# Kernel optimization log

Measured on AMD Instinct MI355X. Metric: run time of the kernel, lower is better.

Reference implementation:

```python
import jax, jax.numpy as jnp
import numpy as np

D_K = 128


def setup_inputs() -> dict:
    key = jax.random.key(0)
    ks = jax.random.split(key, 10)
    B, S, D, TP, TE, DK = 4, 4096, 1024, 16, 64, D_K
    sc = lambda fan_in: 1.0 / np.sqrt(fan_in)
    return {
        "x": jax.random.normal(ks[0], (B, S, D), jnp.float32),
        "time_points": jax.random.normal(ks[1], (B, TP, TE), jnp.float32),
        "Wq": jax.random.normal(ks[2], (D, DK), jnp.float32) * sc(D),
        "bq": jnp.zeros((DK,), jnp.float32),
        "Wk": jax.random.normal(ks[3], (D, DK), jnp.float32) * sc(D),
        "bk": jnp.zeros((DK,), jnp.float32),
        "Wv": jax.random.normal(ks[4], (D, DK), jnp.float32) * sc(D),
        "bv": jnp.zeros((DK,), jnp.float32),
        "Wt": jax.random.normal(ks[5], (TE, DK), jnp.float32) * sc(TE),
        "bt": jnp.zeros((DK,), jnp.float32),
    }


def reference(x, time_points, Wq, bq, Wk, bk, Wv, bv, Wt, bt):
    B, S, _ = x.shape
    Q = x @ Wq + bq              # [B,S,dk]
    K = x @ Wk + bk              # [B,S,dk]
    V = x @ Wv + bv              # [B,S,dk]
    E = time_points @ Wt + bt    # [B,TP,dk] = time_emb
    # T = repeat(E, S times along dim 1). Then T^T @ T = S * E^T E and
    # ||T||_F = sqrt(S) * ||E||_F, so we never materialize T.
    S_f = jnp.asarray(S, jnp.float32)
    EtE = jnp.einsum('btd,bte->bde', E, E)            # [B,dk,dk]
    T_norm = jnp.sqrt(S_f * jnp.sum(E * E, axis=(1, 2), keepdims=False))  # [B]
    T_scaled = (S_f * EtE) / (T_norm[:, None, None] + 1e-8)  # [B,dk,dk]
    QT = jnp.einsum('bsd,bde->bse', Q, T_scaled)      # [B,S,dk]
    scores = jnp.einsum('bse,bte->bst', QT, K)        # [B,S,S]
    scores = scores / jnp.sqrt(jnp.asarray(D_K, jnp.float32))
    attn = jax.nn.softmax(scores, axis=-1)            # [B,S,S]
    out = jnp.einsum('bst,btd->bsd', attn, V)         # [B,S,dk]
    return out, attn
```

## Files before the change

### kernel.cpp

```cpp
#include <hip/hip_runtime.h>
#include <math.h>

#define BB 4
#define SS 4096
#define DD 1024
#define TPp 16
#define TEe 64
#define DKk 128

typedef __attribute__((ext_vector_type(8))) short short8;
typedef __attribute__((ext_vector_type(4))) float floatx4;
typedef __attribute__((ext_vector_type(16))) float floatx16;

#define BSTRIDE 524288
#define WFRAG 131072
#define XTILE 32768

static __device__ inline short f2bf(float f) {
  union { float f; unsigned u; } v; v.f = f;
  unsigned r = v.u + 0x7fff + ((v.u >> 16) & 1);
  return (short)(r >> 16);
}
static __device__ inline float bf2f(short s) {
  union { unsigned u; float f; } v; v.u = ((unsigned)(unsigned short)s) << 16;
  return v.f;
}

__global__ __launch_bounds__(256) void temb_kernel(const float* __restrict__ tp,
                                                   const float* __restrict__ Wt,
                                                   const float* __restrict__ bt,
                                                   const float* __restrict__ bq,
                                                   float* __restrict__ Tws,
                                                   float* __restrict__ bqtws) {
  __shared__ float sE[TPp * DKk];
  __shared__ float sB[TPp];
  __shared__ float red[256];
  const int p = blockIdx.x, b = blockIdx.y;
  const int tid = threadIdx.x;
  float lsq = 0.f;
  for (int l = 0; l < 8; ++l) {
    int idx = tid + 256 * l;
    int i = idx >> 7, j = idx & 127;
    float a = bt[j];
    for (int c = 0; c < TEe; ++c)
      a += tp[((size_t)b * TPp + i) * TEe + c] * Wt[c * DKk + j];
    sE[idx] = a;
    lsq += a * a;
  }
  red[tid] = lsq;
  __syncthreads();
  for (int s2 = 128; s2 > 0; s2 >>= 1) {
    if (tid < s2) red[tid] += red[tid + s2];
    __syncthreads();
  }
  const float total = red[0];
  const float scale = (float)SS / (sqrtf((float)SS * total) + 1e-8f);
  if (tid < TPp) {
    float a = 0.f;
    for (int d2 = 0; d2 < DKk; ++d2) a += bq[d2] * sE[tid * DKk + d2];
    sB[tid] = a;
  }
  __syncthreads();
  for (int l = 0; l < 8; ++l) {
    int idx = p * 2048 + tid + 256 * l;
    int d2 = idx >> 7, e = idx & 127;
    float a = 0.f;
    #pragma unroll
    for (int t = 0; t < TPp; ++t) a += sE[t * DKk + d2] * sE[t * DKk + e];
    Tws[(size_t)b * DKk * DKk + idx] = scale * a;
  }
  if (p == 0 && tid < DKk) {
    float a = 0.f;
    #pragma unroll
    for (int t = 0; t < TPp; ++t) a += sB[t] * sE[t * DKk + tid];
    bqtws[b * DKk + tid] = scale * a;
  }
}

__global__ __launch_bounds__(128) void wqp_kernel(const float* __restrict__ Wq,
                                                  const float* __restrict__ Tws,
                                                  short* __restrict__ WqphF,
                                                  short* __restrict__ WqplF) {
  __shared__ float sW[DKk];
  const int m = blockIdx.x, b = blockIdx.y;
  const int e = threadIdx.x;
  sW[e] = Wq[(size_t)m * DKk + e];
  __syncthreads();
  const float* Tb = Tws + (size_t)b * DKk * DKk;
  float a = 0.f;
  #pragma unroll 8
  for (int d2 = 0; d2 < DKk; ++d2) a += sW[d2] * Tb[d2 * DKk + e];
  const size_t off = (size_t)b * WFRAG +
      (size_t)((e >> 5) * 64 + (m >> 4)) * 512 + (32 * ((m >> 3) & 1) + (e & 31)) * 8 +
      (m & 7);
  short hh = f2bf(a);
  WqphF[off] = hh;
  WqplF[off] = f2bf(a - bf2f(hh));
}

__global__ __launch_bounds__(256) void wcast_kernel(const float* __restrict__ Wk,
                                                    const float* __restrict__ Wv,
                                                    short* __restrict__ WkhF,
                                                    short* __restrict__ WklF,
                                                    short* __restrict__ WvhF,
                                                    short* __restrict__ WvlF) {
  const float* W = blockIdx.y ? Wv : Wk;
  short* H = blockIdx.y ? WvhF : WkhF;
  short* L = blockIdx.y ? WvlF : WklF;
  const int ks = blockIdx.x;
  const int wave = threadIdx.x >> 6, lane = threadIdx.x & 63;
  const int n = wave * 32 + (lane & 31);
  const int k0 = ks * 16 + (lane >> 5) * 8;
  short8 h, l;
  #pragma unroll
  for (int j = 0; j < 8; ++j) {
    float v = W[(size_t)(k0 + j) * DKk + n];
    short hh = f2bf(v);
    h[j] = hh;
    l[j] = f2bf(v - bf2f(hh));
  }
  const size_t off = ((size_t)wave * 64 + ks) * 512 + lane * 8;
  *(short8*)&H[off] = h;
  *(short8*)&L[off] = l;
}

__global__ __launch_bounds__(256) void xcast_kernel(const float* __restrict__ x,
                                                    short* __restrict__ XAh,
                                                    short* __restrict__ XAl) {
  const int tileG = blockIdx.x;
  const int rowbase = tileG * 32;
  const int tid = threadIdx.x;
  const int t = tid & 31, khalf = (tid >> 5) & 1, w = tid >> 6;
  const size_t abase = (size_t)tileG * XTILE + (size_t)(tid & 63) * 8;
  const float* xr = x + (size_t)(rowbase + t) * DD + khalf * 8;
  #pragma unroll
  for (int it = 0; it < 16; ++it) {
    const int ks = it * 4 + w;
    float4 u0 = *(const float4*)(xr + ks * 16);
    float4 u1 = *(const float4*)(xr + ks * 16 + 4);
    const float v[8] = {u0.x, u0.y, u0.z, u0.w, u1.x, u1.y, u1.z, u1.w};
    short8 h, l;
    #pragma unroll
    for (int j = 0; j < 8; ++j) {
      short hh = f2bf(v[j]);
      h[j] = hh;
      l[j] = f2bf(v[j] - bf2f(hh));
    }
    *(short8*)&XAh[abase + (size_t)ks * 512] = h;
    *(short8*)&XAl[abase + (size_t)ks * 512] = l;
  }
}

__global__ __launch_bounds__(256, 4) void proj_kernel(const short* __restrict__ XAh,
                                                      const short* __restrict__ XAl,
                                                      const short* __restrict__ WqphF,
                                                      const short* __restrict__ WqplF,
                                                      const short* __restrict__ WkhF,
                                                      const short* __restrict__ WklF,
                                                      const short* __restrict__ WvhF,
                                                      const short* __restrict__ WvlF,
                                                      const float* __restrict__ bqt,
                                                      const float* __restrict__ bk,
                                                      const float* __restrict__ bv,
                                                      short* __restrict__ QTh,
                                                      short* __restrict__ QTl,
                                                      short* __restrict__ Kh,
                                                      short* __restrict__ Kl,
                                                      short* __restrict__ VT) {
  const int id = blockIdx.x;
  const int region = id >> 9, tileG = id & 511;
  const int b = tileG >> 7, tileL = tileG & 127;
  const int tid = threadIdx.x, wave = tid >> 6, lane = tid & 63;
  const int l31 = lane & 31, half = lane >> 5;
  const short* BH;
  const short* BL;
  if (region == 0)      { BH = WqphF + (size_t)b * WFRAG; BL = WqplF + (size_t)b * WFRAG; }
  else if (region == 1) { BH = WkhF; BL = WklF; }
  else                  { BH = WvhF; BL = WvlF; }
  BH += (size_t)wave * 32768 + (size_t)lane * 8;
  BL += (size_t)wave * 32768 + (size_t)lane * 8;
  const short* AH = XAh + (size_t)tileG * XTILE + (size_t)lane * 8;
  const short* AL = XAl + (size_t)tileG * XTILE + (size_t)lane * 8;
  floatx16 accE, accO;
  #pragma unroll
  for (int r = 0; r < 16; ++r) { accE[r] = 0.f; accO[r] = 0.f; }
  for (int ks = 0; ks < 64; ks += 2) {
    short8 a0h = *(const short8*)(AH + (size_t)ks * 512);
    short8 a0l = *(const short8*)(AL + (size_t)ks * 512);
    short8 b0h = *(const short8*)(BH + (size_t)ks * 512);
    short8 b0l = *(const short8*)(BL + (size_t)ks * 512);
    short8 a1h = *(const short8*)(AH + (size_t)(ks + 1) * 512);
    short8 a1l = *(const short8*)(AL + (size_t)(ks + 1) * 512);
    short8 b1h = *(const short8*)(BH + (size_t)(ks + 1) * 512);
    short8 b1l = *(const short8*)(BL + (size_t)(ks + 1) * 512);
    accE = __builtin_amdgcn_mfma_f32_32x32x16_bf16(a0l, b0h, accE, 0, 0, 0);
    accO = __builtin_amdgcn_mfma_f32_32x32x16_bf16(a1l, b1h, accO, 0, 0, 0);
    accE = __builtin_amdgcn_mfma_f32_32x32x16_bf16(a0h, b0l, accE, 0, 0, 0);
    accO = __builtin_amdgcn_mfma_f32_32x32x16_bf16(a1h, b1l, accO, 0, 0, 0);
    accE = __builtin_amdgcn_mfma_f32_32x32x16_bf16(a0h, b0h, accE, 0, 0, 0);
    accO = __builtin_amdgcn_mfma_f32_32x32x16_bf16(a1h, b1h, accO, 0, 0, 0);
  }
  floatx16 acc;
  #pragma unroll
  for (int r = 0; r < 16; ++r) acc[r] = accE[r] + accO[r];
  const int f = wave * 32 + l31;
  if (region <= 1) {
    short* Hp = (region == 0) ? QTh : Kh;
    short* Lp = (region == 0) ? QTl : Kl;
    const float bias = (region == 0) ? bqt[b * DKk + f] : bk[f];
    const int fks = f >> 4, fh = (f >> 3) & 1, fj = f & 7;
    const size_t qkbase =
        (size_t)b * BSTRIDE + (size_t)tileL * 4096 + (size_t)fks * 512 + fj;
    #pragma unroll
    for (int reg = 0; reg < 16; ++reg) {
      const int t = (reg & 3) + 8 * (reg >> 2) + 4 * half;
      const size_t off = qkbase + (size_t)(fh * 32 + t) * 8;
      float v = acc[reg] + bias;
      short hh = f2bf(v);
      Hp[off] = hh;
      Lp[off] = f2bf(v - bf2f(hh));
    }
  } else {
    const float biasv = bv[f];
    #pragma unroll
    for (int g = 0; g < 4; ++g) {
      short4 s4;
      s4.x = f2bf(acc[4 * g + 0] + biasv);
      s4.y = f2bf(acc[4 * g + 1] + biasv);
      s4.z = f2bf(acc[4 * g + 2] + biasv);
      s4.w = f2bf(acc[4 * g + 3] + biasv);
      const size_t off = (size_t)b * BSTRIDE +
          (size_t)(wave * 256 + tileL * 2 + (g >> 1)) * 512 +
          (size_t)((g & 1) * 32 + l31) * 8 + 4 * half;
      *(short4*)&VT[off] = s4;
    }
  }
}

__global__ __launch_bounds__(256, 2) void ml_kernel(const short* __restrict__ QTh,
                                                    const short* __restrict__ QTl,
                                                    const short* __restrict__ Kh,
                                                    const short* __restrict__ Kl,
                                                    float* __restrict__ mrow,
                                                    float* __restrict__ linv) {
  __shared__ float smM[4][32], smL[4][32];
  const int id = blockIdx.x;
  const int xcd = id & 7;
  const int b = xcd >> 1;
  const int tile = ((id >> 3) << 1) + (xcd & 1);
  const int rowbase = tile * 32;
  const int tid = threadIdx.x;
  const int wave = tid >> 6, lane = tid & 63;
  const int l31 = lane & 31;
  const float sc = 0.088388347648318447f;
  const size_t qbase = (size_t)b * BSTRIDE + (size_t)tile * 4096 + lane * 8;
  short8 qh[8], ql[8];
  #pragma unroll
  for (int ks = 0; ks < 8; ++ks) {
    qh[ks] = *(const short8*)(QTh + qbase + ks * 512);
    ql[ks] = *(const short8*)(QTl + qbase + ks * 512);
  }
  float m = -INFINITY, l = 0.f;
  for (int ct = wave; ct < 128; ct += 4) {
    const size_t kbase = (size_t)b * BSTRIDE + (size_t)ct * 4096 + lane * 8;
    floatx16 accA, accB;
    #pragma unroll
    for (int r = 0; r < 16; ++r) { accA[r] = 0.f; accB[r] = 0.f; }
    #pragma unroll
    for (int ks = 0; ks < 4; ++ks) {
      short8 kh0 = *(const short8*)(Kh + kbase + ks * 512);
      short8 kl0 = *(const short8*)(Kl + kbase + ks * 512);
      short8 kh1 = *(const short8*)(Kh + kbase + (ks + 4) * 512);
      short8 kl1 = *(const short8*)(Kl + kbase + (ks + 4) * 512);
      accA = __builtin_amdgcn_mfma_f32_32x32x16_bf16(kh0, qh[ks], accA, 0, 0, 0);
      accB = __builtin_amdgcn_mfma_f32_32x32x16_bf16(kh1, qh[ks + 4], accB, 0, 0, 0);
      accA = __builtin_amdgcn_mfma_f32_32x32x16_bf16(kh0, ql[ks], accA, 0, 0, 0);
      accB = __builtin_amdgcn_mfma_f32_32x32x16_bf16(kh1, ql[ks + 4], accB, 0, 0, 0);
      accA = __builtin_amdgcn_mfma_f32_32x32x16_bf16(kl0, qh[ks], accA, 0, 0, 0);
      accB = __builtin_amdgcn_mfma_f32_32x32x16_bf16(kl1, qh[ks + 4], accB, 0, 0, 0);
    }
    float s[16];
    float tmax = -INFINITY;
    #pragma unroll
    for (int r = 0; r < 16; ++r) {
      s[r] = (accA[r] + accB[r]) * sc;
      tmax = fmaxf(tmax, s[r]);
    }
    const float mn = fmaxf(m, tmax);
    float ps = 0.f;
    #pragma unroll
    for (int r = 0; r < 16; ++r) ps += __expf(s[r] - mn);
    l = l * __expf(m - mn) + ps;
    m = mn;
  }
  {
    const float mo = __shfl_xor(m, 32, 64);
    const float lo = __shfl_xor(l, 32, 64);
    const float mn = fmaxf(m, mo);
    l = l * __expf(m - mn) + lo * __expf(mo - mn);
    m = mn;
  }
  if (lane < 32) { smM[wave][l31] = m; smL[wave][l31] = l; }
  __syncthreads();
  if (tid < 32) {
    float mm = smM[0][tid], ll = smL[0][tid];
    #pragma unroll
    for (int w = 1; w < 4; ++w) {
      const float mo = smM[w][tid], lo = smL[w][tid];
      const float mn = fmaxf(mm, mo);
      ll = ll * __expf(mm - mn) + lo * __expf(mo - mn);
      mm = mn;
    }
    mrow[b * SS + rowbase + tid] = mm;
    linv[b * SS + rowbase + tid] = 1.0f / ll;
  }
}

__global__ __launch_bounds__(256, 2) void pv_kernel(const short* __restrict__ QTh,
                                                    const short* __restrict__ QTl,
                                                    const short* __restrict__ Kh,
                                                    const short* __restrict__ Kl,
                                                    const short* __restrict__ VT,
                                                    float* __restrict__ attn,
                                                    const float* __restrict__ mrow,
                                                    const float* __restrict__ linv,
                                                    float* __restrict__ outp) {
  __shared__ float sAcc[3][4][64][16];
  const int id = blockIdx.x;
  const int xcd = id & 7;
  const int b = xcd >> 1;
  const int tile = ((id >> 3) << 1) + (xcd & 1);
  const int rowbase = tile * 32;
  const int tid = threadIdx.x;
  const int wave = tid >> 6, lane = tid & 63;
  const int l31 = lane & 31, half = lane >> 5;
  const float sc = 0.088388347648318447f;
  const size_t qbase = (size_t)b * BSTRIDE + (size_t)tile * 4096 + lane * 8;
  short8 qh[8], ql[8];
  #pragma unroll
  for (int ks = 0; ks < 8; ++ks) {
    qh[ks] = *(const short8*)(QTh + qbase + ks * 512);
    ql[ks] = *(const short8*)(QTl + qbase + ks * 512);
  }
  const float m_i = mrow[b * SS + rowbase + l31];
  const float li = linv[b * SS + rowbase + l31];
  float* arow = attn + (size_t)b * SS * SS + (size_t)(rowbase + l31) * SS + 4 * half;
  const short* vtb = VT + (size_t)b * BSTRIDE + lane * 8;
  floatx16 pacc[4];
  #pragma unroll
  for (int dt = 0; dt < 4; ++dt)
    #pragma unroll
    for (int r = 0; r < 16; ++r) pacc[dt][r] = 0.f;
  for (int ct = wave; ct < 128; ct += 4) {
    const size_t kbase = (size_t)b * BSTRIDE + (size_t)ct * 4096 + lane * 8;
    floatx16 accA, accB;
    #pragma unroll
    for (int r = 0; r < 16; ++r) { accA[r] = 0.f; accB[r] = 0.f; }
    #pragma unroll
    for (int ks = 0; ks < 4; ++ks) {
      short8 kh0 = *(const short8*)(Kh + kbase + ks * 512);
      short8 kl0 = *(const short8*)(Kl + kbase + ks * 512);
      short8 kh1 = *(const short8*)(Kh + kbase + (ks + 4) * 512);
      short8 kl1 = *(const short8*)(Kl + kbase + (ks + 4) * 512);
      accA = __builtin_amdgcn_mfma_f32_32x32x16_bf16(kh0, qh[ks], accA, 0, 0, 0);
      accB = __builtin_amdgcn_mfma_f32_32x32x16_bf16(kh1, qh[ks + 4], accB, 0, 0, 0);
      accA = __builtin_amdgcn_mfma_f32_32x32x16_bf16(kh0, ql[ks], accA, 0, 0, 0);
      accB = __builtin_amdgcn_mfma_f32_32x32x16_bf16(kh1, ql[ks + 4], accB, 0, 0, 0);
      accA = __builtin_amdgcn_mfma_f32_32x32x16_bf16(kl0, qh[ks], accA, 0, 0, 0);
      accB = __builtin_amdgcn_mfma_f32_32x32x16_bf16(kl1, qh[ks + 4], accB, 0, 0, 0);
    }
    float p[16];
    #pragma unroll
    for (int r = 0; r < 16; ++r)
      p[r] = __expf((accA[r] + accB[r]) * sc - m_i) * li;
    #pragma unroll
    for (int g = 0; g < 4; ++g) {
      floatx4 o = {p[4 * g], p[4 * g + 1], p[4 * g + 2], p[4 * g + 3]};
      __builtin_nontemporal_store(o, (floatx4*)(arow + ct * 32 + 8 * g));
    }
    short8 af0, af1;
    #pragma unroll
    for (int rr = 0; rr < 4; ++rr) {
      const float shl = __shfl_xor(p[rr], 32, 64);
      const float shh = __shfl_xor(p[rr + 4], 32, 64);
      af0[rr] = f2bf(half ? shh : p[rr]);
      af0[rr + 4] = f2bf(half ? p[rr + 4] : shl);
      const float shl2 = __shfl_xor(p[rr + 8], 32, 64);
      const float shh2 = __shfl_xor(p[rr + 12], 32, 64);
      af1[rr] = f2bf(half ? shh2 : p[rr + 8]);
      af1[rr + 4] = f2bf(half ? p[rr + 12] : shl2);
    }
    #pragma unroll
    for (int dt = 0; dt < 4; ++dt) {
      short8 v0 = *(const short8*)(vtb + (size_t)(dt * 256 + ct * 2) * 512);
      pacc[dt] = __builtin_amdgcn_mfma_f32_32x32x16_bf16(af0, v0, pacc[dt], 0, 0, 0);
      short8 v1 = *(const short8*)(vtb + (size_t)(dt * 256 + ct * 2 + 1) * 512);
      pacc[dt] = __builtin_amdgcn_mfma_f32_32x32x16_bf16(af1, v1, pacc[dt], 0, 0, 0);
    }
  }
  if (wave > 0) {
    #pragma unroll
    for (int dt = 0; dt < 4; ++dt)
      #pragma unroll
      for (int r = 0; r < 16; ++r) sAcc[wave - 1][dt][lane][r] = pacc[dt][r];
  }
  __syncthreads();
  if (wave == 0) {
    #pragma unroll
    for (int dt = 0; dt < 4; ++dt)
      #pragma unroll
      for (int r = 0; r < 16; ++r) {
        const int q = (r & 3) + 8 * (r >> 2) + 4 * half;
        const float v = pacc[dt][r] + sAcc[0][dt][lane][r] + sAcc[1][dt][lane][r] +
                        sAcc[2][dt][lane][r];
        outp[((size_t)b * SS + rowbase + q) * DKk + dt * 32 + l31] = v;
      }
  }
}

extern "C" void kernel_launch(void* const* d_in, const int* in_sizes, int n_in,
                              void* d_out, int out_size, void* d_ws, size_t ws_size,
                              hipStream_t stream) {
  const float* x  = (const float*)d_in[0];
  const float* tp = (const float*)d_in[1];
  const float* Wq = (const float*)d_in[2];
  const float* bq = (const float*)d_in[3];
  const float* Wk = (const float*)d_in[4];
  const float* bk = (const float*)d_in[5];
  const float* Wv = (const float*)d_in[6];
  const float* bv = (const float*)d_in[7];
  const float* Wt = (const float*)d_in[8];
  const float* bt = (const float*)d_in[9];
  float* out  = (float*)d_out;
  float* attn = out + (size_t)BB * SS * DKk;
  float* ws = (float*)d_ws;
  float* Tws   = ws;
  float* bqt   = ws + 65536;
  short* WqphF = (short*)(ws + 66048);
  short* WqplF = (short*)(ws + 328192);
  short* WkhF  = (short*)(ws + 590336);
  short* WklF  = (short*)(ws + 655872);
  short* WvhF  = (short*)(ws + 721408);
  short* WvlF  = (short*)(ws + 786944);
  short* XAh   = (short*)(ws + 852480);
  short* XAl   = (short*)(ws + 9241088);
  short* QTh   = (short*)(ws + 17629696);
  short* QTl   = (short*)(ws + 18678272);
  short* Kh    = (short*)(ws + 19726848);
  short* Kl    = (short*)(ws + 20775424);
  short* VT    = (short*)(ws + 21824000);
  float* mrow  = ws + 22872576;
  float* lin   = ws + 22888960;

  temb_kernel<<<dim3(8, 4), 256, 0, stream>>>(tp, Wt, bt, bq, Tws, bqt);
  wqp_kernel<<<dim3(1024, 4), 128, 0, stream>>>(Wq, Tws, WqphF, WqplF);
  wcast_kernel<<<dim3(64, 2), 256, 0, stream>>>(Wk, Wv, WkhF, WklF, WvhF, WvlF);
  xcast_kernel<<<512, 256, 0, stream>>>(x, XAh, XAl);
  proj_kernel<<<1536, 256, 0, stream>>>(XAh, XAl, WqphF, WqplF, WkhF, WklF,
                                        WvhF, WvlF, bqt, bk, bv,
                                        QTh, QTl, Kh, Kl, VT);
  ml_kernel<<<512, 256, 0, stream>>>(QTh, QTl, Kh, Kl, mrow, lin);
  pv_kernel<<<512, 256, 0, stream>>>(QTh, QTl, Kh, Kl, VT, attn, mrow, lin, out);
}
```

Measured before the change: 620.0 us.

## Fuse QKV projections per tile and split attention key range across blocks

```diff
diff --git a/kernel.cpp b/kernel.cpp
--- a/kernel.cpp
+++ b/kernel.cpp
@@ -151,7 +151,7 @@
   }
 }
 
-__global__ __launch_bounds__(256, 4) void proj_kernel(const short* __restrict__ XAh,
+__global__ __launch_bounds__(256, 2) void proj_kernel(const short* __restrict__ XAh,
                                                       const short* __restrict__ XAl,
                                                       const short* __restrict__ WqphF,
                                                       const short* __restrict__ WqplF,
@@ -167,73 +167,73 @@
                                                       short* __restrict__ Kh,
                                                       short* __restrict__ Kl,
                                                       short* __restrict__ VT) {
-  const int id = blockIdx.x;
-  const int region = id >> 9, tileG = id & 511;
+  const int tileG = blockIdx.x;
   const int b = tileG >> 7, tileL = tileG & 127;
   const int tid = threadIdx.x, wave = tid >> 6, lane = tid & 63;
   const int l31 = lane & 31, half = lane >> 5;
-  const short* BH;
-  const short* BL;
-  if (region == 0)      { BH = WqphF + (size_t)b * WFRAG; BL = WqplF + (size_t)b * WFRAG; }
-  else if (region == 1) { BH = WkhF; BL = WklF; }
-  else                  { BH = WvhF; BL = WvlF; }
-  BH += (size_t)wave * 32768 + (size_t)lane * 8;
-  BL += (size_t)wave * 32768 + (size_t)lane * 8;
+  const size_t woff = (size_t)wave * 32768 + (size_t)lane * 8;
+  const short* BQh = WqphF + (size_t)b * WFRAG + woff;
+  const short* BQl = WqplF + (size_t)b * WFRAG + woff;
+  const short* BKh = WkhF + woff;
+  const short* BKl = WklF + woff;
+  const short* BVh = WvhF + woff;
+  const short* BVl = WvlF + woff;
   const short* AH = XAh + (size_t)tileG * XTILE + (size_t)lane * 8;
   const short* AL = XAl + (size_t)tileG * XTILE + (size_t)lane * 8;
-  floatx16 accE, accO;
-  #pragma unroll
-  for (int r = 0; r < 16; ++r) { accE[r] = 0.f; accO[r] = 0.f; }
-  for (int ks = 0; ks < 64; ks += 2) {
-    short8 a0h = *(const short8*)(AH + (size_t)ks * 512);
-    short8 a0l = *(const short8*)(AL + (size_t)ks * 512);
-    short8 b0h = *(const short8*)(BH + (size_t)ks * 512);
-    short8 b0l = *(const short8*)(BL + (size_t)ks * 512);
-    short8 a1h = *(const short8*)(AH + (size_t)(ks + 1) * 512);
-    short8 a1l = *(const short8*)(AL + (size_t)(ks + 1) * 512);
-    short8 b1h = *(const short8*)(BH + (size_t)(ks + 1) * 512);
-    short8 b1l = *(const short8*)(BL + (size_t)(ks + 1) * 512);
-    accE = __builtin_amdgcn_mfma_f32_32x32x16_bf16(a0l, b0h, accE, 0, 0, 0);
-    accO = __builtin_amdgcn_mfma_f32_32x32x16_bf16(a1l, b1h, accO, 0, 0, 0);
-    accE = __builtin_amdgcn_mfma_f32_32x32x16_bf16(a0h, b0l, accE, 0, 0, 0);
-    accO = __builtin_amdgcn_mfma_f32_32x32x16_bf16(a1h, b1l, accO, 0, 0, 0);
-    accE = __builtin_amdgcn_mfma_f32_32x32x16_bf16(a0h, b0h, accE, 0, 0, 0);
-    accO = __builtin_amdgcn_mfma_f32_32x32x16_bf16(a1h, b1h, accO, 0, 0, 0);
-  }
-  floatx16 acc;
-  #pragma unroll
-  for (int r = 0; r < 16; ++r) acc[r] = accE[r] + accO[r];
+  floatx16 acc0, acc1, acc2;
+  #pragma unroll
+  for (int r = 0; r < 16; ++r) { acc0[r] = 0.f; acc1[r] = 0.f; acc2[r] = 0.f; }
+  for (int ks = 0; ks < 64; ++ks) {
+    const size_t o = (size_t)ks * 512;
+    short8 ah = *(const short8*)(AH + o);
+    short8 al = *(const short8*)(AL + o);
+    short8 bh0 = *(const short8*)(BQh + o);
+    short8 bl0 = *(const short8*)(BQl + o);
+    short8 bh1 = *(const short8*)(BKh + o);
+    short8 bl1 = *(const short8*)(BKl + o);
+    short8 bh2 = *(const short8*)(BVh + o);
+    short8 bl2 = *(const short8*)(BVl + o);
+    acc0 = __builtin_amdgcn_mfma_f32_32x32x16_bf16(al, bh0, acc0, 0, 0, 0);
+    acc1 = __builtin_amdgcn_mfma_f32_32x32x16_bf16(al, bh1, acc1, 0, 0, 0);
+    acc2 = __builtin_amdgcn_mfma_f32_32x32x16_bf16(al, bh2, acc2, 0, 0, 0);
+    acc0 = __builtin_amdgcn_mfma_f32_32x32x16_bf16(ah, bl0, acc0, 0, 0, 0);
+    acc1 = __builtin_amdgcn_mfma_f32_32x32x16_bf16(ah, bl1, acc1, 0, 0, 0);
+    acc2 = __builtin_amdgcn_mfma_f32_32x32x16_bf16(ah, bl2, acc2, 0, 0, 0);
+    acc0 = __builtin_amdgcn_mfma_f32_32x32x16_bf16(ah, bh0, acc0, 0, 0, 0);
+    acc1 = __builtin_amdgcn_mfma_f32_32x32x16_bf16(ah, bh1, acc1, 0, 0, 0);
+    acc2 = __builtin_amdgcn_mfma_f32_32x32x16_bf16(ah, bh2, acc2, 0, 0, 0);
+  }
   const int f = wave * 32 + l31;
-  if (region <= 1) {
-    short* Hp = (region == 0) ? QTh : Kh;
-    short* Lp = (region == 0) ? QTl : Kl;
-    const float bias = (region == 0) ? bqt[b * DKk + f] : bk[f];
-    const int fks = f >> 4, fh = (f >> 3) & 1, fj = f & 7;
-    const size_t qkbase =
-        (size_t)b * BSTRIDE + (size_t)tileL * 4096 + (size_t)fks * 512 + fj;
-    #pragma unroll
-    for (int reg = 0; reg < 16; ++reg) {
-      const int t = (reg & 3) + 8 * (reg >> 2) + 4 * half;
-      const size_t off = qkbase + (size_t)(fh * 32 + t) * 8;
-      float v = acc[reg] + bias;
-      short hh = f2bf(v);
-      Hp[off] = hh;
-      Lp[off] = f2bf(v - bf2f(hh));
-    }
-  } else {
-    const float biasv = bv[f];
-    #pragma unroll
-    for (int g = 0; g < 4; ++g) {
-      short4 s4;
-      s4.x = f2bf(acc[4 * g + 0] + biasv);
-      s4.y = f2bf(acc[4 * g + 1] + biasv);
-      s4.z = f2bf(acc[4 * g + 2] + biasv);
-      s4.w = f2bf(acc[4 * g + 3] + biasv);
-      const size_t off = (size_t)b * BSTRIDE +
-          (size_t)(wave * 256 + tileL * 2 + (g >> 1)) * 512 +
-          (size_t)((g & 1) * 32 + l31) * 8 + 4 * half;
-      *(short4*)&VT[off] = s4;
-    }
+  const int fks = f >> 4, fh = (f >> 3) & 1, fj = f & 7;
+  const size_t qkbase =
+      (size_t)b * BSTRIDE + (size_t)tileL * 4096 + (size_t)fks * 512 + fj;
+  const float biasq = bqt[b * DKk + f];
+  const float biask = bk[f];
+  #pragma unroll
+  for (int reg = 0; reg < 16; ++reg) {
+    const int t = (reg & 3) + 8 * (reg >> 2) + 4 * half;
+    const size_t off = qkbase + (size_t)(fh * 32 + t) * 8;
+    float v = acc0[reg] + biasq;
+    short hh = f2bf(v);
+    QTh[off] = hh;
+    QTl[off] = f2bf(v - bf2f(hh));
+    v = acc1[reg] + biask;
+    hh = f2bf(v);
+    Kh[off] = hh;
+    Kl[off] = f2bf(v - bf2f(hh));
+  }
+  const float biasv = bv[f];
+  #pragma unroll
+  for (int g = 0; g < 4; ++g) {
+    short4 s4;
+    s4.x = f2bf(acc2[4 * g + 0] + biasv);
+    s4.y = f2bf(acc2[4 * g + 1] + biasv);
+    s4.z = f2bf(acc2[4 * g + 2] + biasv);
+    s4.w = f2bf(acc2[4 * g + 3] + biasv);
+    const size_t off = (size_t)b * BSTRIDE +
+        (size_t)(wave * 256 + tileL * 2 + (g >> 1)) * 512 +
+        (size_t)((g & 1) * 32 + l31) * 8 + 4 * half;
+    *(short4*)&VT[off] = s4;
   }
 }
 
@@ -241,19 +241,17 @@
                                                     const short* __restrict__ QTl,
                                                     const short* __restrict__ Kh,
                                                     const short* __restrict__ Kl,
-                                                    float* __restrict__ mrow,
-                                                    float* __restrict__ linv) {
-  __shared__ float smM[4][32], smL[4][32];
+                                                    float* __restrict__ mlP) {
   const int id = blockIdx.x;
-  const int xcd = id & 7;
-  const int b = xcd >> 1;
-  const int tile = ((id >> 3) << 1) + (xcd & 1);
-  const int rowbase = tile * 32;
+  const int s = id & 3;
+  const int b = (id >> 2) & 3;
+  const int rg = id >> 4;
   const int tid = threadIdx.x;
   const int wave = tid >> 6, lane = tid & 63;
   const int l31 = lane & 31;
+  const int qtile = rg * 4 + wave;
   const float sc = 0.088388347648318447f;
-  const size_t qbase = (size_t)b * BSTRIDE + (size_t)tile * 4096 + lane * 8;
+  const size_t qbase = (size_t)b * BSTRIDE + (size_t)qtile * 4096 + lane * 8;
   short8 qh[8], ql[8];
   #pragma unroll
   for (int ks = 0; ks < 8; ++ks) {
@@ -261,7 +259,8 @@
     ql[ks] = *(const short8*)(QTl + qbase + ks * 512);
   }
   float m = -INFINITY, l = 0.f;
-  for (int ct = wave; ct < 128; ct += 4) {
+  for (int i = 0; i < 32; ++i) {
+    const int ct = s * 32 + i;
     const size_t kbase = (size_t)b * BSTRIDE + (size_t)ct * 4096 + lane * 8;
     floatx16 accA, accB;
     #pragma unroll
@@ -279,17 +278,17 @@
       accA = __builtin_amdgcn_mfma_f32_32x32x16_bf16(kl0, qh[ks], accA, 0, 0, 0);
       accB = __builtin_amdgcn_mfma_f32_32x32x16_bf16(kl1, qh[ks + 4], accB, 0, 0, 0);
     }
-    float s[16];
+    float sv[16];
     float tmax = -INFINITY;
     #pragma unroll
     for (int r = 0; r < 16; ++r) {
-      s[r] = (accA[r] + accB[r]) * sc;
-      tmax = fmaxf(tmax, s[r]);
+      sv[r] = (accA[r] + accB[r]) * sc;
+      tmax = fmaxf(tmax, sv[r]);
     }
     const float mn = fmaxf(m, tmax);
     float ps = 0.f;
     #pragma unroll
-    for (int r = 0; r < 16; ++r) ps += __expf(s[r] - mn);
+    for (int r = 0; r < 16; ++r) ps += __expf(sv[r] - mn);
     l = l * __expf(m - mn) + ps;
     m = mn;
   }
@@ -300,20 +299,28 @@
     l = l * __expf(m - mn) + lo * __expf(mo - mn);
     m = mn;
   }
-  if (lane < 32) { smM[wave][l31] = m; smL[wave][l31] = l; }
-  __syncthreads();
-  if (tid < 32) {
-    float mm = smM[0][tid], ll = smL[0][tid];
-    #pragma unroll
-    for (int w = 1; w < 4; ++w) {
-      const float mo = smM[w][tid], lo = smL[w][tid];
-      const float mn = fmaxf(mm, mo);
-      ll = ll * __expf(mm - mn) + lo * __expf(mo - mn);
-      mm = mn;
-    }
-    mrow[b * SS + rowbase + tid] = mm;
-    linv[b * SS + rowbase + tid] = 1.0f / ll;
-  }
+  if (lane < 32) {
+    const int q = b * SS + qtile * 32 + l31;
+    mlP[(s * 2 + 0) * (BB * SS) + q] = m;
+    mlP[(s * 2 + 1) * (BB * SS) + q] = l;
+  }
+}
+
+__global__ __launch_bounds__(256) void mlred_kernel(const float* __restrict__ mlP,
+                                                    float* __restrict__ mrow,
+                                                    float* __restrict__ linv) {
+  const int q = blockIdx.x * 256 + threadIdx.x;
+  float m = mlP[q], l = mlP[BB * SS + q];
+  #pragma unroll
+  for (int s = 1; s < 4; ++s) {
+    const float mo = mlP[(s * 2 + 0) * (BB * SS) + q];
+    const float lo = mlP[(s * 2 + 1) * (BB * SS) + q];
+    const float mn = fmaxf(m, mo);
+    l = l * __expf(m - mn) + lo * __expf(mo - mn);
+    m = mn;
+  }
+  mrow[q] = m;
+  linv[q] = 1.0f / l;
 }
 
 __global__ __launch_bounds__(256, 2) void pv_kernel(const short* __restrict__ QTh,
@@ -324,34 +331,34 @@
                                                     float* __restrict__ attn,
                                                     const float* __restrict__ mrow,
                                                     const float* __restrict__ linv,
-                                                    float* __restrict__ outp) {
-  __shared__ float sAcc[3][4][64][16];
+                                                    float* __restrict__ outP) {
   const int id = blockIdx.x;
-  const int xcd = id & 7;
-  const int b = xcd >> 1;
-  const int tile = ((id >> 3) << 1) + (xcd & 1);
-  const int rowbase = tile * 32;
+  const int s = id & 3;
+  const int b = (id >> 2) & 3;
+  const int rg = id >> 4;
   const int tid = threadIdx.x;
   const int wave = tid >> 6, lane = tid & 63;
   const int l31 = lane & 31, half = lane >> 5;
+  const int qtile = rg * 4 + wave;
   const float sc = 0.088388347648318447f;
-  const size_t qbase = (size_t)b * BSTRIDE + (size_t)tile * 4096 + lane * 8;
+  const size_t qbase = (size_t)b * BSTRIDE + (size_t)qtile * 4096 + lane * 8;
   short8 qh[8], ql[8];
   #pragma unroll
   for (int ks = 0; ks < 8; ++ks) {
     qh[ks] = *(const short8*)(QTh + qbase + ks * 512);
     ql[ks] = *(const short8*)(QTl + qbase + ks * 512);
   }
-  const float m_i = mrow[b * SS + rowbase + l31];
-  const float li = linv[b * SS + rowbase + l31];
-  float* arow = attn + (size_t)b * SS * SS + (size_t)(rowbase + l31) * SS + 4 * half;
+  const float m_i = mrow[b * SS + qtile * 32 + l31];
+  const float li = linv[b * SS + qtile * 32 + l31];
+  float* arow = attn + (size_t)b * SS * SS + (size_t)(qtile * 32 + l31) * SS + 4 * half;
   const short* vtb = VT + (size_t)b * BSTRIDE + lane * 8;
   floatx16 pacc[4];
   #pragma unroll
   for (int dt = 0; dt < 4; ++dt)
     #pragma unroll
     for (int r = 0; r < 16; ++r) pacc[dt][r] = 0.f;
-  for (int ct = wave; ct < 128; ct += 4) {
+  for (int i = 0; i < 32; ++i) {
+    const int ct = s * 32 + i;
     const size_t kbase = (size_t)b * BSTRIDE + (size_t)ct * 4096 + lane * 8;
     floatx16 accA, accB;
     #pragma unroll
@@ -376,7 +383,7 @@
     #pragma unroll
     for (int g = 0; g < 4; ++g) {
       floatx4 o = {p[4 * g], p[4 * g + 1], p[4 * g + 2], p[4 * g + 3]};
-      __builtin_nontemporal_store(o, (floatx4*)(arow + ct * 32 + 8 * g));
+      *(floatx4*)(arow + ct * 32 + 8 * g) = o;
     }
     short8 af0, af1;
     #pragma unroll
@@ -398,24 +405,26 @@
       pacc[dt] = __builtin_amdgcn_mfma_f32_32x32x16_bf16(af1, v1, pacc[dt], 0, 0, 0);
     }
   }
-  if (wave > 0) {
-    #pragma unroll
-    for (int dt = 0; dt < 4; ++dt)
-      #pragma unroll
-      for (int r = 0; r < 16; ++r) sAcc[wave - 1][dt][lane][r] = pacc[dt][r];
-  }
-  __syncthreads();
-  if (wave == 0) {
-    #pragma unroll
-    for (int dt = 0; dt < 4; ++dt)
-      #pragma unroll
-      for (int r = 0; r < 16; ++r) {
-        const int q = (r & 3) + 8 * (r >> 2) + 4 * half;
-        const float v = pacc[dt][r] + sAcc[0][dt][lane][r] + sAcc[1][dt][lane][r] +
-                        sAcc[2][dt][lane][r];
-        outp[((size_t)b * SS + rowbase + q) * DKk + dt * 32 + l31] = v;
-      }
-  }
+  float* op = outP + (size_t)s * (BB * SS * DKk);
+  #pragma unroll
+  for (int dt = 0; dt < 4; ++dt)
+    #pragma unroll
+    for (int r = 0; r < 16; ++r) {
+      const int qloc = (r & 3) + 8 * (r >> 2) + 4 * half;
+      op[((size_t)b * SS + qtile * 32 + qloc) * DKk + dt * 32 + l31] = pacc[dt][r];
+    }
+}
+
+__global__ __launch_bounds__(256) void outred_kernel(const float* __restrict__ outP,
+                                                     float* __restrict__ outp) {
+  const size_t idx = ((size_t)blockIdx.x * 256 + threadIdx.x) * 4;
+  const size_t N = (size_t)BB * SS * DKk;
+  floatx4 a0 = *(const floatx4*)(outP + idx);
+  floatx4 a1 = *(const floatx4*)(outP + N + idx);
+  floatx4 a2 = *(const floatx4*)(outP + 2 * N + idx);
+  floatx4 a3 = *(const floatx4*)(outP + 3 * N + idx);
+  floatx4 r = a0 + a1 + a2 + a3;
+  *(floatx4*)(outp + idx) = r;
 }
 
 extern "C" void kernel_launch(void* const* d_in, const int* in_sizes, int n_in,
@@ -451,14 +460,18 @@
   short* VT    = (short*)(ws + 21824000);
   float* mrow  = ws + 22872576;
   float* lin   = ws + 22888960;
+  float* mlP   = ws + 22905344;
+  float* outP  = ws + 23036416;
 
   temb_kernel<<<dim3(8, 4), 256, 0, stream>>>(tp, Wt, bt, bq, Tws, bqt);
   wqp_kernel<<<dim3(1024, 4), 128, 0, stream>>>(Wq, Tws, WqphF, WqplF);
   wcast_kernel<<<dim3(64, 2), 256, 0, stream>>>(Wk, Wv, WkhF, WklF, WvhF, WvlF);
   xcast_kernel<<<512, 256, 0, stream>>>(x, XAh, XAl);
-  proj_kernel<<<1536, 256, 0, stream>>>(XAh, XAl, WqphF, WqplF, WkhF, WklF,
-                                        WvhF, WvlF, bqt, bk, bv,
-                                        QTh, QTl, Kh, Kl, VT);
-  ml_kernel<<<512, 256, 0, stream>>>(QTh, QTl, Kh, Kl, mrow, lin);
-  pv_kernel<<<512, 256, 0, stream>>>(QTh, QTl, Kh, Kl, VT, attn, mrow, lin, out);
-}
+  proj_kernel<<<512, 256, 0, stream>>>(XAh, XAl, WqphF, WqplF, WkhF, WklF,
+                                       WvhF, WvlF, bqt, bk, bv,
+                                       QTh, QTl, Kh, Kl, VT);
+  ml_kernel<<<512, 256, 0, stream>>>(QTh, QTl, Kh, Kl, mlP);
+  mlred_kernel<<<64, 256, 0, stream>>>(mlP, mrow, lin);
+  pv_kernel<<<512, 256, 0, stream>>>(QTh, QTl, Kh, Kl, VT, attn, mrow, lin, outP);
+  outred_kernel<<<2048, 256, 0, stream>>>(outP, out);
+}
```

New measurement: 647.4 us. 4.4% more time.
